# Performance work log

Hardware: AMD Instinct MI355X
Metric: run time of the kernel (lower is better)

The kernel has to match this reference:

```python
import jax, jax.numpy as jnp
import numpy as np

K = 3          # kernel size
KF = K * K     # kernel field = 9
PAD = 1
STRIDE = 1


def _conv(x, w, b):
    y = jax.lax.conv_general_dilated(
        x, w, (STRIDE, STRIDE), [(PAD, PAD), (PAD, PAD)],
        dimension_numbers=('NCHW', 'OIHW', 'NCHW'))
    return y + b[None, :, None, None]


def _bilinear_gather(x, py, px):
    # x: [B,C,H,W]; py/px: [B,KF,Ho,Wo] float sampling coords (zero-pad outside)
    B, C, H, W = x.shape
    xf = x.reshape(B, C, H * W)
    y0 = jnp.floor(py)
    x0 = jnp.floor(px)

    def corner(yc, xc):
        wy = 1.0 - jnp.abs(py - yc)
        wx = 1.0 - jnp.abs(px - xc)
        valid = (yc >= 0) & (yc <= H - 1) & (xc >= 0) & (xc <= W - 1)
        yi = jnp.clip(yc, 0, H - 1).astype(jnp.int32)
        xi = jnp.clip(xc, 0, W - 1).astype(jnp.int32)
        idx = (yi * W + xi).reshape(B, -1)               # [B, KF*Ho*Wo]
        v = jax.vmap(lambda f, i: f[:, i])(xf, idx)      # [B, C, KF*Ho*Wo]
        wgt = (wy * wx * valid.astype(x.dtype)).reshape(B, 1, -1)
        return v * wgt

    return (corner(y0, x0) + corner(y0, x0 + 1) +
            corner(y0 + 1, x0) + corner(y0 + 1, x0 + 1))  # [B,C,KF*Ho*Wo]


def _deform_conv(x, offset, mask, w, b):
    # modulated deformable conv v2 (mmcv offset layout: [y,x] interleaved per kernel pt)
    B, C, H, W = x.shape
    Ho, Wo = mask.shape[2], mask.shape[3]
    kh, kw = jnp.meshgrid(jnp.arange(K), jnp.arange(K), indexing='ij')
    kh = kh.reshape(-1).astype(x.dtype)   # [KF]
    kw = kw.reshape(-1).astype(x.dtype)
    base_y = (jnp.arange(Ho) * STRIDE - PAD).astype(x.dtype)
    base_x = (jnp.arange(Wo) * STRIDE - PAD).astype(x.dtype)
    off = offset.reshape(B, KF, 2, Ho, Wo)
    py = base_y[None, None, :, None] + kh[None, :, None, None] + off[:, :, 0]
    px = base_x[None, None, None, :] + kw[None, :, None, None] + off[:, :, 1]
    val = _bilinear_gather(x, py, px).reshape(B, C, KF, Ho, Wo)
    val = val * mask[:, None]                             # modulate
    out = jnp.einsum('bckhw,ock->bohw', val, w.reshape(w.shape[0], C, KF))
    return out + b[None, :, None, None]


def setup_inputs() -> dict:
    key = jax.random.key(0)
    k1, k2, k3 = jax.random.split(key, 3)
    B, C, H, W = 8, 64, 128, 128
    x = jax.random.normal(k1, (B, C, H, W), dtype=jnp.float32)
    w_om = jax.random.normal(k2, (3 * KF, C, K, K), dtype=jnp.float32) * 0.02
    b_om = jnp.zeros((3 * KF,), dtype=jnp.float32)
    w_dc = jax.random.normal(k3, (64, C, K, K), dtype=jnp.float32) * 0.05
    b_dc = jnp.zeros((64,), dtype=jnp.float32)
    return {"x": x, "w_om": w_om, "b_om": b_om, "w_dc": w_dc, "b_dc": b_dc}


def reference(x, w_om, b_om, w_dc, b_dc):
    om = _conv(x, w_om, b_om)                 # [B, 3*KF, H, W]
    offset = om[:, :2 * KF]
    mask = 2.0 * jax.nn.sigmoid(om[:, 2 * KF:])
    return _deform_conv(x, offset, mask, w_dc, b_dc)
```

## Files before the change

kernel.cpp:

```cpp
#include <hip/hip_runtime.h>
#include <cmath>

#define IH 128
#define IW 128
#define NB 8

typedef __attribute__((ext_vector_type(8))) short bf16x8;
typedef __attribute__((ext_vector_type(4))) float f32x4;
typedef __attribute__((ext_vector_type(2))) float f32x2;

union U4B8 { uint4 u; bf16x8 h; };

#define OFFM_OFF 0
#define XT_OFF   3538944
#define WTDC_OFF (3538944 + 4194304)
#define WTOM_OFF (3538944 + 4194304 + 18432)

__device__ __forceinline__ unsigned short f32_to_bf16(float f) {
    unsigned int u = __float_as_uint(f);
    u += 0x7fffu + ((u >> 16) & 1u);
    return (unsigned short)(u >> 16);
}

__global__ void transpose_weights(const float* __restrict__ w_dc,
                                  const float* __restrict__ w_om,
                                  unsigned short* __restrict__ wt_dc16,
                                  unsigned short* __restrict__ wt_om16) {
    int idx = blockIdx.x * blockDim.x + threadIdx.x;
    if (idx < 9 * 64 * 64) {
        int k = idx >> 12;
        int o = (idx >> 6) & 63;
        int c = idx & 63;
        wt_dc16[idx] = f32_to_bf16(w_dc[(o * 64 + c) * 9 + k]);
    }
    if (idx < 9 * 32 * 64) {
        int k = idx >> 11;
        int o = (idx >> 6) & 31;
        int c = idx & 63;
        wt_om16[idx] = (o < 27) ? f32_to_bf16(w_om[(o * 64 + c) * 9 + k])
                                : (unsigned short)0;
    }
}

__global__ __launch_bounds__(256) void transpose_x(
        const float* __restrict__ x, unsigned short* __restrict__ xT) {
    __shared__ float t[64 * 65];
    const int tid = threadIdx.x;
    const int blk = blockIdx.x;
    const int b = blk >> 8;
    const int rem = blk & 255;
    const int h = rem >> 1;
    const int w0 = (rem & 1) << 6;

    for (int i = tid; i < 4096; i += 256) {
        const int c = i >> 6;
        const int w = i & 63;
        t[w * 65 + c] = x[(((size_t)(b * 64 + c)) << 14) + (h << 7) + w0 + w];
    }
    __syncthreads();
    const int c2 = (tid & 31) * 2;
    ushort2* dst = (ushort2*)(xT + (((size_t)b << 20)) + ((size_t)((h << 7) + w0)) * 64 + c2);
#pragma unroll
    for (int p = 0; p < 8; ++p) {
        const int w = (tid >> 5) + p * 8;
        ushort2 u;
        u.x = f32_to_bf16(t[w * 65 + c2]);
        u.y = f32_to_bf16(t[w * 65 + c2 + 1]);
        dst[(size_t)w * 32] = u;
    }
}

__global__ __launch_bounds__(256) void conv_om_mfma(
        const unsigned short* __restrict__ xT,
        const float* __restrict__ b_om,
        const unsigned short* __restrict__ wt_om16,
        float* __restrict__ offm) {
    __shared__ __align__(16) unsigned short win[198 * 72];
    __shared__ __align__(16) unsigned short wks[2][32 * 72];

    const int tid = threadIdx.x;
    const int bid = blockIdx.x;
    const int swz = ((bid & 7) << 8) + (bid >> 3);
    const int b = swz >> 8;
    const int rem = swz & 255;
    const int h = rem >> 1;
    const int w0 = (rem & 1) << 6;
    const int wid = tid >> 6;
    const int lane = tid & 63;
    const int ln15 = lane & 15;
    const int quad = lane >> 4;

    for (int idx = tid; idx < 1584; idx += 256) {
        const int pos = idx >> 3;
        const int part = idx & 7;
        const int r = pos / 66;
        const int xx = pos - r * 66;
        const int y = h + r - 1;
        const int xg = w0 + xx - 1;
        uint4 v = make_uint4(0u, 0u, 0u, 0u);
        if (y >= 0 && y < IH && xg >= 0 && xg < IW)
            v = *(const uint4*)(xT + (((size_t)b << 20) + (((y << 7) + xg) << 6) + (part << 3)));
        *(uint4*)&win[pos * 72 + part * 8] = v;
    }
    {
        const int o = tid >> 3;
        const int part = tid & 7;
        *(uint4*)&wks[0][o * 72 + part * 8] =
            *(const uint4*)(wt_om16 + (o << 6) + (part << 3));
    }
    __syncthreads();

    f32x4 acc[2] = {{0.f, 0.f, 0.f, 0.f}, {0.f, 0.f, 0.f, 0.f}};

    for (int k = 0; k < 9; ++k) {
        const int buf = k & 1;
        if (k < 8) {
            const int o = tid >> 3;
            const int part = tid & 7;
            *(uint4*)&wks[buf ^ 1][o * 72 + part * 8] =
                *(const uint4*)(wt_om16 + ((k + 1) << 11) + (o << 6) + (part << 3));
        }
        const int kh = k / 3;
        const int kw = k - kh * 3;
        const int posb = kh * 66 + wid * 16 + ln15 + kw;
        const unsigned short* wb = wks[buf];
#pragma unroll
        for (int ch = 0; ch < 2; ++ch) {
            const int c = (ch << 5) + (quad << 3);
            U4B8 a, b0, b1;
            a.u  = *(const uint4*)&win[posb * 72 + c];
            b0.u = *(const uint4*)&wb[ln15 * 72 + c];
            b1.u = *(const uint4*)&wb[(16 + ln15) * 72 + c];
            acc[0] = __builtin_amdgcn_mfma_f32_16x16x32_bf16(a.h, b0.h, acc[0], 0, 0, 0);
            acc[1] = __builtin_amdgcn_mfma_f32_16x16x32_bf16(a.h, b1.h, acc[1], 0, 0, 0);
        }
        __syncthreads();
    }

    const int px0 = wid * 16 + quad * 4;
#pragma unroll
    for (int ot = 0; ot < 2; ++ot) {
        const int o = (ot << 4) + ln15;
        if (o >= 27) continue;
        const float bias = b_om[o];
        float4 r;
        r.x = acc[ot][0] + bias;
        r.y = acc[ot][1] + bias;
        r.z = acc[ot][2] + bias;
        r.w = acc[ot][3] + bias;
        if (o >= 18) {
            r.x = 2.0f / (1.0f + __expf(-r.x));
            r.y = 2.0f / (1.0f + __expf(-r.y));
            r.z = 2.0f / (1.0f + __expf(-r.z));
            r.w = 2.0f / (1.0f + __expf(-r.w));
        }
        *(float4*)&offm[(((size_t)(b * 27 + o)) << 14) + (h << 7) + w0 + px0] = r;
    }
}

__device__ __forceinline__ void issue_gather(
        const unsigned short* __restrict__ xb, const float* __restrict__ offs,
        int k, int lpx, int h, int w0, int quad, uint4* g, float* cw) {
    const float offy = offs[(k << 1) * 64 + lpx];
    const float offx = offs[((k << 1) + 1) * 64 + lpx];
    const float msk  = offs[(18 + k) * 64 + lpx];
    const int kh = k / 3;
    const int kw = k - kh * 3;
    const float py  = (float)(h + kh - 1) + offy;
    const float pxf = (float)(w0 + lpx + kw - 1) + offx;
    const float y0f = floorf(py);
    const float x0f = floorf(pxf);
    const float fy = py - y0f;
    const float fx = pxf - x0f;
    const float wy0 = 1.0f - fy, wx0 = 1.0f - fx;
    const float vy0 = (y0f >= 0.0f && y0f <= 127.0f) ? 1.0f : 0.0f;
    const float vy1 = (y0f >= -1.0f && y0f <= 126.0f) ? 1.0f : 0.0f;
    const float vx0 = (x0f >= 0.0f && x0f <= 127.0f) ? 1.0f : 0.0f;
    const float vx1 = (x0f >= -1.0f && x0f <= 126.0f) ? 1.0f : 0.0f;
    cw[0] = wy0 * wx0 * vy0 * vx0 * msk;
    cw[1] = wy0 * fx  * vy0 * vx1 * msk;
    cw[2] = fy  * wx0 * vy1 * vx0 * msk;
    cw[3] = fy  * fx  * vy1 * vx1 * msk;
    const int y0i = min(max((int)y0f, 0), 127);
    const int y1i = min(max((int)y0f + 1, 0), 127);
    const int x0i = min(max((int)x0f, 0), 127);
    const int x1i = min(max((int)x0f + 1, 0), 127);
    const int cofs = quad << 3;
    const unsigned short* p00 = xb + ((((size_t)((y0i << 7) + x0i)) << 6) + cofs);
    const unsigned short* p01 = xb + ((((size_t)((y0i << 7) + x1i)) << 6) + cofs);
    const unsigned short* p10 = xb + ((((size_t)((y1i << 7) + x0i)) << 6) + cofs);
    const unsigned short* p11 = xb + ((((size_t)((y1i << 7) + x1i)) << 6) + cofs);
    g[0] = *(const uint4*)p00;  g[1] = *(const uint4*)(p00 + 32);
    g[2] = *(const uint4*)p01;  g[3] = *(const uint4*)(p01 + 32);
    g[4] = *(const uint4*)p10;  g[5] = *(const uint4*)(p10 + 32);
    g[6] = *(const uint4*)p11;  g[7] = *(const uint4*)(p11 + 32);
}

__device__ __forceinline__ void pack_frags(const uint4* g, const float* cw,
                                           U4B8& a0, U4B8& a1) {
    f32x2 v2[8];
#pragma unroll
    for (int i = 0; i < 8; ++i) v2[i] = (f32x2){0.f, 0.f};
#pragma unroll
    for (int c = 0; c < 4; ++c) {
        f32x2 w2;
        w2.x = cw[c];
        w2.y = cw[c];
        const uint4 ga = g[2 * c];
        const uint4 gb = g[2 * c + 1];
        const unsigned int u[8] = {ga.x, ga.y, ga.z, ga.w, gb.x, gb.y, gb.z, gb.w};
#pragma unroll
        for (int i = 0; i < 8; ++i) {
            f32x2 x2;
            x2.x = __uint_as_float(u[i] << 16);
            x2.y = __uint_as_float(u[i] & 0xffff0000u);
            asm("v_pk_fma_f32 %0, %1, %2, %0" : "+v"(v2[i]) : "v"(x2), "v"(w2));
        }
    }
    unsigned int pk[8];
#pragma unroll
    for (int i = 0; i < 8; ++i)
        asm("v_cvt_pk_bf16_f32 %0, %1, %2"
            : "=v"(pk[i]) : "v"(v2[i].x), "v"(v2[i].y));
    a0.u = make_uint4(pk[0], pk[1], pk[2], pk[3]);
    a1.u = make_uint4(pk[4], pk[5], pk[6], pk[7]);
}

__global__ __launch_bounds__(256) void deform_mfma(
        const unsigned short* __restrict__ xT,
        const float* __restrict__ b_dc,
        const float* __restrict__ offm,
        const unsigned short* __restrict__ wt_dc16,
        float* __restrict__ out) {
    __shared__ __align__(16) float offs[27 * 64];
    __shared__ __align__(16) unsigned short wks[2][64 * 72];

    const int tid = threadIdx.x;
    const int bid = blockIdx.x;
    const int swz = ((bid & 7) << 8) + (bid >> 3);
    const int b = swz >> 8;
    const int rem = swz & 255;
    const int h = rem >> 1;
    const int w0 = (rem & 1) << 6;
    const int wid = tid >> 6;
    const int lane = tid & 63;
    const int ln15 = lane & 15;
    const int quad = lane >> 4;
    const int lpx = (wid << 4) + ln15;

    const int so0 = tid >> 3, sp0 = tid & 7;
    const int so1 = (tid + 256) >> 3, sp1 = tid & 7;

    for (int i = tid; i < 1728; i += 256) {
        offs[i] = offm[(((size_t)(b * 27 + (i >> 6))) << 14) + (h << 7) + w0 + (i & 63)];
    }
    *(uint4*)&wks[0][so0 * 72 + sp0 * 8] = *(const uint4*)(wt_dc16 + (so0 << 6) + (sp0 << 3));
    *(uint4*)&wks[0][so1 * 72 + sp1 * 8] = *(const uint4*)(wt_dc16 + (so1 << 6) + (sp1 << 3));
    __syncthreads();

    const unsigned short* xb = xT + ((size_t)b << 20);

    f32x4 acc[4];
#pragma unroll
    for (int i = 0; i < 4; ++i) acc[i] = (f32x4){0.f, 0.f, 0.f, 0.f};

    uint4 g[2][8];
    float cw[2][4];
    issue_gather(xb, offs, 0, lpx, h, w0, quad, g[0], cw[0]);

#pragma unroll
    for (int k = 0; k < 9; ++k) {
        const int cur = k & 1;
        const int nxt = cur ^ 1;
        if (k < 8) {
            const uint4 wv0 = *(const uint4*)(wt_dc16 + ((k + 1) << 12) + (so0 << 6) + (sp0 << 3));
            const uint4 wv1 = *(const uint4*)(wt_dc16 + ((k + 1) << 12) + (so1 << 6) + (sp1 << 3));
            issue_gather(xb, offs, k + 1, lpx, h, w0, quad, g[nxt], cw[nxt]);
            *(uint4*)&wks[nxt][so0 * 72 + sp0 * 8] = wv0;
            *(uint4*)&wks[nxt][so1 * 72 + sp1 * 8] = wv1;
        }
        U4B8 a0, a1;
        pack_frags(g[cur], cw[cur], a0, a1);
        const unsigned short* wb = wks[cur];
#pragma unroll
        for (int ot = 0; ot < 4; ++ot) {
            U4B8 b0, b1;
            const unsigned short* base = &wb[((ot << 4) + ln15) * 72 + (quad << 3)];
            b0.u = *(const uint4*)base;
            b1.u = *(const uint4*)(base + 32);
            acc[ot] = __builtin_amdgcn_mfma_f32_16x16x32_bf16(a0.h, b0.h, acc[ot], 0, 0, 0);
            acc[ot] = __builtin_amdgcn_mfma_f32_16x16x32_bf16(a1.h, b1.h, acc[ot], 0, 0, 0);
        }
        if (k < 8) {
            asm volatile("s_waitcnt lgkmcnt(0)" ::: "memory");
            __builtin_amdgcn_s_barrier();
            __builtin_amdgcn_sched_barrier(0);
        }
    }

#pragma unroll
    for (int ot = 0; ot < 4; ++ot) {
        const int o = (ot << 4) + ln15;
        const float bias = b_dc[o];
        float4 r;
        r.x = acc[ot][0] + bias;
        r.y = acc[ot][1] + bias;
        r.z = acc[ot][2] + bias;
        r.w = acc[ot][3] + bias;
        *(float4*)&out[(((size_t)(b * 64 + o)) << 14) + (h << 7) + w0 + (wid << 4) + (quad << 2)] = r;
    }
}

extern "C" void kernel_launch(void* const* d_in, const int* in_sizes, int n_in,
                              void* d_out, int out_size, void* d_ws, size_t ws_size,
                              hipStream_t stream) {
    const float* x    = (const float*)d_in[0];
    const float* w_om = (const float*)d_in[1];
    const float* b_om = (const float*)d_in[2];
    const float* w_dc = (const float*)d_in[3];
    const float* b_dc = (const float*)d_in[4];
    float* out = (float*)d_out;
    float* ws  = (float*)d_ws;

    float* offm = ws + OFFM_OFF;
    unsigned short* xT      = (unsigned short*)(ws + XT_OFF);
    unsigned short* wt_dc16 = (unsigned short*)(ws + WTDC_OFF);
    unsigned short* wt_om16 = (unsigned short*)(ws + WTOM_OFF);

    const int n_blocks = NB * IH * (IW / 64);

    transpose_weights<<<144, 256, 0, stream>>>(w_dc, w_om, wt_dc16, wt_om16);
    transpose_x<<<NB * IH * 2, 256, 0, stream>>>(x, xT);
    conv_om_mfma<<<n_blocks, 256, 0, stream>>>(xT, b_om, wt_om16, offm);
    deform_mfma<<<n_blocks, 256, 0, stream>>>(xT, b_dc, offm, wt_dc16, out);
}
```

Measured before the change: 177.6 us.

## Fuse offset/mask conv into deformable conv kernel, keep offsets in LDS

Merges the offset/mask convolution kernel into the deformable-conv kernel. Each block now computes its 27 offset/mask channels with MFMA from direct global loads of the input and weights, instead of staging a halo window in LDS. The results are written to a padded LDS array rather than round-tripping through a global offm buffer. This removes one kernel launch and the global write and read of the offset tensor. The cost is more registers, global loads that are not shared across waves, and a longer critical path per block.

```diff
diff --git a/kernel.cpp b/kernel.cpp
--- a/kernel.cpp
+++ b/kernel.cpp
@@ -70,100 +70,12 @@
     }
 }
 
-__global__ __launch_bounds__(256) void conv_om_mfma(
-        const unsigned short* __restrict__ xT,
-        const float* __restrict__ b_om,
-        const unsigned short* __restrict__ wt_om16,
-        float* __restrict__ offm) {
-    __shared__ __align__(16) unsigned short win[198 * 72];
-    __shared__ __align__(16) unsigned short wks[2][32 * 72];
-
-    const int tid = threadIdx.x;
-    const int bid = blockIdx.x;
-    const int swz = ((bid & 7) << 8) + (bid >> 3);
-    const int b = swz >> 8;
-    const int rem = swz & 255;
-    const int h = rem >> 1;
-    const int w0 = (rem & 1) << 6;
-    const int wid = tid >> 6;
-    const int lane = tid & 63;
-    const int ln15 = lane & 15;
-    const int quad = lane >> 4;
-
-    for (int idx = tid; idx < 1584; idx += 256) {
-        const int pos = idx >> 3;
-        const int part = idx & 7;
-        const int r = pos / 66;
-        const int xx = pos - r * 66;
-        const int y = h + r - 1;
-        const int xg = w0 + xx - 1;
-        uint4 v = make_uint4(0u, 0u, 0u, 0u);
-        if (y >= 0 && y < IH && xg >= 0 && xg < IW)
-            v = *(const uint4*)(xT + (((size_t)b << 20) + (((y << 7) + xg) << 6) + (part << 3)));
-        *(uint4*)&win[pos * 72 + part * 8] = v;
-    }
-    {
-        const int o = tid >> 3;
-        const int part = tid & 7;
-        *(uint4*)&wks[0][o * 72 + part * 8] =
-            *(const uint4*)(wt_om16 + (o << 6) + (part << 3));
-    }
-    __syncthreads();
-
-    f32x4 acc[2] = {{0.f, 0.f, 0.f, 0.f}, {0.f, 0.f, 0.f, 0.f}};
-
-    for (int k = 0; k < 9; ++k) {
-        const int buf = k & 1;
-        if (k < 8) {
-            const int o = tid >> 3;
-            const int part = tid & 7;
-            *(uint4*)&wks[buf ^ 1][o * 72 + part * 8] =
-                *(const uint4*)(wt_om16 + ((k + 1) << 11) + (o << 6) + (part << 3));
-        }
-        const int kh = k / 3;
-        const int kw = k - kh * 3;
-        const int posb = kh * 66 + wid * 16 + ln15 + kw;
-        const unsigned short* wb = wks[buf];
-#pragma unroll
-        for (int ch = 0; ch < 2; ++ch) {
-            const int c = (ch << 5) + (quad << 3);
-            U4B8 a, b0, b1;
-            a.u  = *(const uint4*)&win[posb * 72 + c];
-            b0.u = *(const uint4*)&wb[ln15 * 72 + c];
-            b1.u = *(const uint4*)&wb[(16 + ln15) * 72 + c];
-            acc[0] = __builtin_amdgcn_mfma_f32_16x16x32_bf16(a.h, b0.h, acc[0], 0, 0, 0);
-            acc[1] = __builtin_amdgcn_mfma_f32_16x16x32_bf16(a.h, b1.h, acc[1], 0, 0, 0);
-        }
-        __syncthreads();
-    }
-
-    const int px0 = wid * 16 + quad * 4;
-#pragma unroll
-    for (int ot = 0; ot < 2; ++ot) {
-        const int o = (ot << 4) + ln15;
-        if (o >= 27) continue;
-        const float bias = b_om[o];
-        float4 r;
-        r.x = acc[ot][0] + bias;
-        r.y = acc[ot][1] + bias;
-        r.z = acc[ot][2] + bias;
-        r.w = acc[ot][3] + bias;
-        if (o >= 18) {
-            r.x = 2.0f / (1.0f + __expf(-r.x));
-            r.y = 2.0f / (1.0f + __expf(-r.y));
-            r.z = 2.0f / (1.0f + __expf(-r.z));
-            r.w = 2.0f / (1.0f + __expf(-r.w));
-        }
-        *(float4*)&offm[(((size_t)(b * 27 + o)) << 14) + (h << 7) + w0 + px0] = r;
-    }
-}
-
 __device__ __forceinline__ void issue_gather(
-        const unsigned short* __restrict__ xb, const float* __restrict__ offs,
+        const unsigned short* __restrict__ xb, const float* offs,
         int k, int lpx, int h, int w0, int quad, uint4* g, float* cw) {
-    const float offy = offs[(k << 1) * 64 + lpx];
-    const float offx = offs[((k << 1) + 1) * 64 + lpx];
-    const float msk  = offs[(18 + k) * 64 + lpx];
+    const float offy = offs[(k << 1) * 65 + lpx];
+    const float offx = offs[((k << 1) + 1) * 65 + lpx];
+    const float msk  = offs[(18 + k) * 65 + lpx];
     const int kh = k / 3;
     const int kw = k - kh * 3;
     const float py  = (float)(h + kh - 1) + offy;
@@ -226,13 +138,14 @@
     a1.u = make_uint4(pk[4], pk[5], pk[6], pk[7]);
 }
 
-__global__ __launch_bounds__(256) void deform_mfma(
+__global__ __launch_bounds__(256) void om_deform_fused(
         const unsigned short* __restrict__ xT,
+        const float* __restrict__ b_om,
+        const unsigned short* __restrict__ wt_om16,
         const float* __restrict__ b_dc,
-        const float* __restrict__ offm,
         const unsigned short* __restrict__ wt_dc16,
         float* __restrict__ out) {
-    __shared__ __align__(16) float offs[27 * 64];
+    __shared__ __align__(16) float offs[27 * 65];
     __shared__ __align__(16) unsigned short wks[2][64 * 72];
 
     const int tid = threadIdx.x;
@@ -248,36 +161,113 @@
     const int quad = lane >> 4;
     const int lpx = (wid << 4) + ln15;
 
-    const int so0 = tid >> 3, sp0 = tid & 7;
-    const int so1 = (tid + 256) >> 3, sp1 = tid & 7;
-
-    for (int i = tid; i < 1728; i += 256) {
-        offs[i] = offm[(((size_t)(b * 27 + (i >> 6))) << 14) + (h << 7) + w0 + (i & 63)];
-    }
-    *(uint4*)&wks[0][so0 * 72 + sp0 * 8] = *(const uint4*)(wt_dc16 + (so0 << 6) + (sp0 << 3));
-    *(uint4*)&wks[0][so1 * 72 + sp1 * 8] = *(const uint4*)(wt_dc16 + (so1 << 6) + (sp1 << 3));
-    __syncthreads();
-
     const unsigned short* xb = xT + ((size_t)b << 20);
 
-    f32x4 acc[4];
-#pragma unroll
-    for (int i = 0; i < 4; ++i) acc[i] = (f32x4){0.f, 0.f, 0.f, 0.f};
-
-    uint4 g[2][8];
-    float cw[2][4];
-    issue_gather(xb, offs, 0, lpx, h, w0, quad, g[0], cw[0]);
-
+    f32x4 oacc[2] = {{0.f, 0.f, 0.f, 0.f}, {0.f, 0.f, 0.f, 0.f}};
+    uint4 pa[2][2];
+    int   pav[2];
+    uint4 pb[2][4];
+
+#define ISSUE_A(K, S)                                                         \
+    {                                                                         \
+        const int kh_ = (K) / 3, kw_ = (K) - kh_ * 3;                         \
+        const int y_ = h + kh_ - 1;                                           \
+        const int xg_ = w0 + lpx + kw_ - 1;                                   \
+        pav[S] = (y_ >= 0 && y_ < IH && xg_ >= 0 && xg_ < IW);                \
+        const int yc_ = min(max(y_, 0), IH - 1);                              \
+        const int xc_ = min(max(xg_, 0), IW - 1);                             \
+        const unsigned short* p_ =                                            \
+            xb + ((((size_t)((yc_ << 7) + xc_)) << 6) + (quad << 3));         \
+        pa[S][0] = *(const uint4*)p_;                                         \
+        pa[S][1] = *(const uint4*)(p_ + 32);                                  \
+    }
+#define ISSUE_B(K, S)                                                         \
+    {                                                                         \
+        const unsigned short* wg_ = wt_om16 + ((K) << 11) + (quad << 3);      \
+        const unsigned short* q0_ = wg_ + (ln15 << 6);                        \
+        const unsigned short* q1_ = wg_ + ((16 + ln15) << 6);                 \
+        pb[S][0] = *(const uint4*)q0_;                                        \
+        pb[S][1] = *(const uint4*)(q0_ + 32);                                 \
+        pb[S][2] = *(const uint4*)q1_;                                        \
+        pb[S][3] = *(const uint4*)(q1_ + 32);                                 \
+    }
+
+    ISSUE_B(0, 0)
+    ISSUE_A(0, 0)
 #pragma unroll
     for (int k = 0; k < 9; ++k) {
         const int cur = k & 1;
         const int nxt = cur ^ 1;
         if (k < 8) {
-            const uint4 wv0 = *(const uint4*)(wt_dc16 + ((k + 1) << 12) + (so0 << 6) + (sp0 << 3));
-            const uint4 wv1 = *(const uint4*)(wt_dc16 + ((k + 1) << 12) + (so1 << 6) + (sp1 << 3));
+            ISSUE_B(k + 1, nxt)
+            ISSUE_A(k + 1, nxt)
+        }
+        const uint4 z = make_uint4(0u, 0u, 0u, 0u);
+        U4B8 a0, a1, b00, b01, b10, b11;
+        a0.u = pav[cur] ? pa[cur][0] : z;
+        a1.u = pav[cur] ? pa[cur][1] : z;
+        b00.u = pb[cur][0];
+        b01.u = pb[cur][1];
+        b10.u = pb[cur][2];
+        b11.u = pb[cur][3];
+        oacc[0] = __builtin_amdgcn_mfma_f32_16x16x32_bf16(a0.h, b00.h, oacc[0], 0, 0, 0);
+        oacc[0] = __builtin_amdgcn_mfma_f32_16x16x32_bf16(a1.h, b01.h, oacc[0], 0, 0, 0);
+        oacc[1] = __builtin_amdgcn_mfma_f32_16x16x32_bf16(a0.h, b10.h, oacc[1], 0, 0, 0);
+        oacc[1] = __builtin_amdgcn_mfma_f32_16x16x32_bf16(a1.h, b11.h, oacc[1], 0, 0, 0);
+    }
+#undef ISSUE_A
+#undef ISSUE_B
+
+    const int so0 = tid >> 3, sp = tid & 7;
+    const int so1 = so0 + 32;
+    {
+        const uint4 wv0 = *(const uint4*)(wt_dc16 + (so0 << 6) + (sp << 3));
+        const uint4 wv1 = *(const uint4*)(wt_dc16 + (so1 << 6) + (sp << 3));
+        *(uint4*)&wks[0][so0 * 72 + sp * 8] = wv0;
+        *(uint4*)&wks[0][so1 * 72 + sp * 8] = wv1;
+    }
+
+    const int px0 = (wid << 4) + (quad << 2);
+#pragma unroll
+    for (int ot = 0; ot < 2; ++ot) {
+        const int o = (ot << 4) + ln15;
+        if (o < 27) {
+            const float bias = b_om[o];
+            float r[4];
+            r[0] = oacc[ot][0] + bias;
+            r[1] = oacc[ot][1] + bias;
+            r[2] = oacc[ot][2] + bias;
+            r[3] = oacc[ot][3] + bias;
+            if (o >= 18) {
+#pragma unroll
+                for (int j = 0; j < 4; ++j)
+                    r[j] = 2.0f / (1.0f + __expf(-r[j]));
+            }
+#pragma unroll
+            for (int j = 0; j < 4; ++j)
+                offs[o * 65 + px0 + j] = r[j];
+        }
+    }
+    __syncthreads();
+
+    f32x4 acc[4];
+#pragma unroll
+    for (int i = 0; i < 4; ++i) acc[i] = (f32x4){0.f, 0.f, 0.f, 0.f};
+
+    uint4 g[2][8];
+    float cw[2][4];
+    issue_gather(xb, offs, 0, lpx, h, w0, quad, g[0], cw[0]);
+
+#pragma unroll
+    for (int k = 0; k < 9; ++k) {
+        const int cur = k & 1;
+        const int nxt = cur ^ 1;
+        if (k < 8) {
+            const uint4 wv0 = *(const uint4*)(wt_dc16 + ((k + 1) << 12) + (so0 << 6) + (sp << 3));
+            const uint4 wv1 = *(const uint4*)(wt_dc16 + ((k + 1) << 12) + (so1 << 6) + (sp << 3));
             issue_gather(xb, offs, k + 1, lpx, h, w0, quad, g[nxt], cw[nxt]);
-            *(uint4*)&wks[nxt][so0 * 72 + sp0 * 8] = wv0;
-            *(uint4*)&wks[nxt][so1 * 72 + sp1 * 8] = wv1;
+            *(uint4*)&wks[nxt][so0 * 72 + sp * 8] = wv0;
+            *(uint4*)&wks[nxt][so1 * 72 + sp * 8] = wv1;
         }
         U4B8 a0, a1;
         pack_frags(g[cur], cw[cur], a0, a1);
@@ -322,7 +312,6 @@
     float* out = (float*)d_out;
     float* ws  = (float*)d_ws;
 
-    float* offm = ws + OFFM_OFF;
     unsigned short* xT      = (unsigned short*)(ws + XT_OFF);
     unsigned short* wt_dc16 = (unsigned short*)(ws + WTDC_OFF);
     unsigned short* wt_om16 = (unsigned short*)(ws + WTOM_OFF);
@@ -331,6 +320,5 @@
 
     transpose_weights<<<144, 256, 0, stream>>>(w_dc, w_om, wt_dc16, wt_om16);
     transpose_x<<<NB * IH * 2, 256, 0, stream>>>(x, xT);
-    conv_om_mfma<<<n_blocks, 256, 0, stream>>>(xT, b_om, wt_om16, offm);
-    deform_mfma<<<n_blocks, 256, 0, stream>>>(xT, b_dc, offm, wt_dc16, out);
-}
+    om_deform_fused<<<n_blocks, 256, 0, stream>>>(xT, b_om, wt_om16, b_dc, wt_dc16, out);
+}
```

New measurement: 202.7 us. 14.1% more time.

## Widen deform and transpose blocks to full image rows with vectorized transpose

Applied to the files above, without the earlier changes.

The deformable-conv kernel now processes a full 128-pixel row per block with 512 threads (8 waves), halving the block count so each staged weight tile is shared by twice as many pixels. The offset/mask staging buffer is padded to a stride of 129. The x transpose also handles a full row per block, using float4 global loads and packed bf16 conversion with 16-byte stores. The larger blocks use more LDS and registers per block, which may reduce occupancy.

```diff
diff --git a/kernel.cpp b/kernel.cpp
--- a/kernel.cpp
+++ b/kernel.cpp
@@ -4,6 +4,7 @@
 #define IH 128
 #define IW 128
 #define NB 8
+#define OFFS_STRIDE 129
 
 typedef __attribute__((ext_vector_type(8))) short bf16x8;
 typedef __attribute__((ext_vector_type(4))) float f32x4;
@@ -44,29 +45,35 @@
 
 __global__ __launch_bounds__(256) void transpose_x(
         const float* __restrict__ x, unsigned short* __restrict__ xT) {
-    __shared__ float t[64 * 65];
+    __shared__ __align__(16) float t[64][132];
     const int tid = threadIdx.x;
-    const int blk = blockIdx.x;
-    const int b = blk >> 8;
-    const int rem = blk & 255;
-    const int h = rem >> 1;
-    const int w0 = (rem & 1) << 6;
-
-    for (int i = tid; i < 4096; i += 256) {
-        const int c = i >> 6;
-        const int w = i & 63;
-        t[w * 65 + c] = x[(((size_t)(b * 64 + c)) << 14) + (h << 7) + w0 + w];
+    const int b = blockIdx.x >> 7;
+    const int h = blockIdx.x & 127;
+
+#pragma unroll
+    for (int j = 0; j < 8; ++j) {
+        const int i = (j << 8) + tid;
+        const int c = i >> 5;
+        const int w4 = i & 31;
+        const float4 v = *(const float4*)&x[(((size_t)(b * 64 + c)) << 14) + (h << 7) + (w4 << 2)];
+        *(float4*)&t[c][w4 << 2] = v;
     }
     __syncthreads();
-    const int c2 = (tid & 31) * 2;
-    ushort2* dst = (ushort2*)(xT + (((size_t)b << 20)) + ((size_t)((h << 7) + w0)) * 64 + c2);
-#pragma unroll
-    for (int p = 0; p < 8; ++p) {
-        const int w = (tid >> 5) + p * 8;
-        ushort2 u;
-        u.x = f32_to_bf16(t[w * 65 + c2]);
-        u.y = f32_to_bf16(t[w * 65 + c2 + 1]);
-        dst[(size_t)w * 32] = u;
+
+#pragma unroll
+    for (int j = 0; j < 4; ++j) {
+        const int u = (j << 8) + tid;
+        const int px = u & 127;
+        const int cg = u >> 7;
+        unsigned int pk[4];
+#pragma unroll
+        for (int e = 0; e < 4; ++e) {
+            const float lo = t[(cg << 3) + 2 * e][px];
+            const float hi = t[(cg << 3) + 2 * e + 1][px];
+            asm("v_cvt_pk_bf16_f32 %0, %1, %2" : "=v"(pk[e]) : "v"(lo), "v"(hi));
+        }
+        *(uint4*)(xT + (((size_t)b << 20) + ((size_t)((h << 7) + px) << 6) + (cg << 3))) =
+            make_uint4(pk[0], pk[1], pk[2], pk[3]);
     }
 }
 
@@ -159,15 +166,15 @@
 }
 
 __device__ __forceinline__ void issue_gather(
-        const unsigned short* __restrict__ xb, const float* __restrict__ offs,
-        int k, int lpx, int h, int w0, int quad, uint4* g, float* cw) {
-    const float offy = offs[(k << 1) * 64 + lpx];
-    const float offx = offs[((k << 1) + 1) * 64 + lpx];
-    const float msk  = offs[(18 + k) * 64 + lpx];
+        const unsigned short* __restrict__ xb, const float* offs,
+        int k, int lpx, int h, int quad, uint4* g, float* cw) {
+    const float offy = offs[(k << 1) * OFFS_STRIDE + lpx];
+    const float offx = offs[((k << 1) + 1) * OFFS_STRIDE + lpx];
+    const float msk  = offs[(18 + k) * OFFS_STRIDE + lpx];
     const int kh = k / 3;
     const int kw = k - kh * 3;
     const float py  = (float)(h + kh - 1) + offy;
-    const float pxf = (float)(w0 + lpx + kw - 1) + offx;
+    const float pxf = (float)(lpx + kw - 1) + offx;
     const float y0f = floorf(py);
     const float x0f = floorf(pxf);
     const float fy = py - y0f;
@@ -226,36 +233,35 @@
     a1.u = make_uint4(pk[4], pk[5], pk[6], pk[7]);
 }
 
-__global__ __launch_bounds__(256) void deform_mfma(
+__global__ __launch_bounds__(512) void deform_mfma(
         const unsigned short* __restrict__ xT,
         const float* __restrict__ b_dc,
         const float* __restrict__ offm,
         const unsigned short* __restrict__ wt_dc16,
         float* __restrict__ out) {
-    __shared__ __align__(16) float offs[27 * 64];
+    __shared__ __align__(16) float offs[27 * OFFS_STRIDE];
     __shared__ __align__(16) unsigned short wks[2][64 * 72];
 
     const int tid = threadIdx.x;
     const int bid = blockIdx.x;
-    const int swz = ((bid & 7) << 8) + (bid >> 3);
-    const int b = swz >> 8;
-    const int rem = swz & 255;
-    const int h = rem >> 1;
-    const int w0 = (rem & 1) << 6;
+    const int swz = ((bid & 7) << 7) + (bid >> 3);
+    const int b = swz >> 7;
+    const int h = swz & 127;
     const int wid = tid >> 6;
     const int lane = tid & 63;
     const int ln15 = lane & 15;
     const int quad = lane >> 4;
     const int lpx = (wid << 4) + ln15;
 
-    const int so0 = tid >> 3, sp0 = tid & 7;
-    const int so1 = (tid + 256) >> 3, sp1 = tid & 7;
-
-    for (int i = tid; i < 1728; i += 256) {
-        offs[i] = offm[(((size_t)(b * 27 + (i >> 6))) << 14) + (h << 7) + w0 + (i & 63)];
-    }
-    *(uint4*)&wks[0][so0 * 72 + sp0 * 8] = *(const uint4*)(wt_dc16 + (so0 << 6) + (sp0 << 3));
-    *(uint4*)&wks[0][so1 * 72 + sp1 * 8] = *(const uint4*)(wt_dc16 + (so1 << 6) + (sp1 << 3));
+    for (int i = tid; i < 27 * 128; i += 512) {
+        const int ch = i >> 7;
+        const int px = i & 127;
+        offs[ch * OFFS_STRIDE + px] =
+            offm[(((size_t)(b * 27 + ch)) << 14) + (h << 7) + px];
+    }
+    const int so = tid >> 3, sp = tid & 7;
+    *(uint4*)&wks[0][so * 72 + sp * 8] =
+        *(const uint4*)(wt_dc16 + (so << 6) + (sp << 3));
     __syncthreads();
 
     const unsigned short* xb = xT + ((size_t)b << 20);
@@ -266,18 +272,16 @@
 
     uint4 g[2][8];
     float cw[2][4];
-    issue_gather(xb, offs, 0, lpx, h, w0, quad, g[0], cw[0]);
+    issue_gather(xb, offs, 0, lpx, h, quad, g[0], cw[0]);
 
 #pragma unroll
     for (int k = 0; k < 9; ++k) {
         const int cur = k & 1;
         const int nxt = cur ^ 1;
         if (k < 8) {
-            const uint4 wv0 = *(const uint4*)(wt_dc16 + ((k + 1) << 12) + (so0 << 6) + (sp0 << 3));
-            const uint4 wv1 = *(const uint4*)(wt_dc16 + ((k + 1) << 12) + (so1 << 6) + (sp1 << 3));
-            issue_gather(xb, offs, k + 1, lpx, h, w0, quad, g[nxt], cw[nxt]);
-            *(uint4*)&wks[nxt][so0 * 72 + sp0 * 8] = wv0;
-            *(uint4*)&wks[nxt][so1 * 72 + sp1 * 8] = wv1;
+            const uint4 wv = *(const uint4*)(wt_dc16 + ((k + 1) << 12) + (so << 6) + (sp << 3));
+            issue_gather(xb, offs, k + 1, lpx, h, quad, g[nxt], cw[nxt]);
+            *(uint4*)&wks[nxt][so * 72 + sp * 8] = wv;
         }
         U4B8 a0, a1;
         pack_frags(g[cur], cw[cur], a0, a1);
@@ -307,7 +311,7 @@
         r.y = acc[ot][1] + bias;
         r.z = acc[ot][2] + bias;
         r.w = acc[ot][3] + bias;
-        *(float4*)&out[(((size_t)(b * 64 + o)) << 14) + (h << 7) + w0 + (wid << 4) + (quad << 2)] = r;
+        *(float4*)&out[(((size_t)(b * 64 + o)) << 14) + (h << 7) + (wid << 4) + (quad << 2)] = r;
     }
 }
 
@@ -327,10 +331,8 @@
     unsigned short* wt_dc16 = (unsigned short*)(ws + WTDC_OFF);
     unsigned short* wt_om16 = (unsigned short*)(ws + WTOM_OFF);
 
-    const int n_blocks = NB * IH * (IW / 64);
-
     transpose_weights<<<144, 256, 0, stream>>>(w_dc, w_om, wt_dc16, wt_om16);
-    transpose_x<<<NB * IH * 2, 256, 0, stream>>>(x, xT);
-    conv_om_mfma<<<n_blocks, 256, 0, stream>>>(xT, b_om, wt_om16, offm);
-    deform_mfma<<<n_blocks, 256, 0, stream>>>(xT, b_dc, offm, wt_dc16, out);
-}
+    transpose_x<<<NB * IH, 256, 0, stream>>>(x, xT);
+    conv_om_mfma<<<NB * IH * 2, 256, 0, stream>>>(xT, b_om, wt_om16, offm);
+    deform_mfma<<<NB * IH, 512, 0, stream>>>(xT, b_dc, offm, wt_dc16, out);
+}
```

Result: no change. 181.0 us (+1.9%).
